# Performance work log

Hardware: AMD Instinct MI355X
Metric: run time of the kernel (lower is better)

## Reference

```python
import jax, jax.numpy as jnp
import numpy as np

N = 33_554_432
NUM_CLASSES = 10


def setup_inputs() -> dict:
    key = jax.random.key(0)
    k1, k2, k3 = jax.random.split(key, 3)
    predictions = jax.random.normal(k1, (N,), dtype=jnp.float32)
    labels = jax.random.randint(k2, (N,), 0, NUM_CLASSES, dtype=jnp.int32)
    weights = jax.random.uniform(k3, (NUM_CLASSES,), dtype=jnp.float32)
    return {"predictions": predictions, "labels": labels, "weights": weights}


def reference(predictions, labels, weights):
    # per-element weighted squared error: weights[label] * (pred - label)^2, then mean
    diff = predictions - labels.astype(predictions.dtype)
    w = weights[labels]  # gather per-class weight
    return jnp.mean(w * diff * diff)
```

## Files before the change

kernel.cpp:

```cpp
#include <hip/hip_runtime.h>

#define NBLOCKS 2048
#define NTHREADS 256
#define PER_THREAD 16
#define BATCH 4

__global__ __launch_bounds__(NTHREADS) void wmse_kernel(
    const float4* __restrict__ pred4,
    const int4* __restrict__ lab4,
    const float* __restrict__ weights,
    float* __restrict__ out,
    int n4, double inv_n)
{
    __shared__ float w[16];
    if (threadIdx.x < 10) w[threadIdx.x] = weights[threadIdx.x];
    __syncthreads();

    const int stride = NBLOCKS * NTHREADS;
    const int base = blockIdx.x * NTHREADS + threadIdx.x;

    double acc = 0.0;

    if (n4 == stride * PER_THREAD) {
        #pragma unroll 1
        for (int b = 0; b < PER_THREAD / BATCH; ++b) {
            float4 p[BATCH];
            int4   l[BATCH];
            #pragma unroll
            for (int k = 0; k < BATCH; ++k) {
                int i = base + (b * BATCH + k) * stride;
                p[k] = pred4[i];
                l[k] = lab4[i];
            }
            float s = 0.f;
            #pragma unroll
            for (int k = 0; k < BATCH; ++k) {
                float d0 = p[k].x - (float)l[k].x;
                float d1 = p[k].y - (float)l[k].y;
                float d2 = p[k].z - (float)l[k].z;
                float d3 = p[k].w - (float)l[k].w;
                s += w[l[k].x] * d0 * d0;
                s += w[l[k].y] * d1 * d1;
                s += w[l[k].z] * d2 * d2;
                s += w[l[k].w] * d3 * d3;
            }
            acc += (double)s;
        }
    } else {
        for (int i = base; i < n4; i += stride) {
            float4 p = pred4[i];
            int4 l = lab4[i];
            float d0 = p.x - (float)l.x;
            float d1 = p.y - (float)l.y;
            float d2 = p.z - (float)l.z;
            float d3 = p.w - (float)l.w;
            float s = w[l.x] * d0 * d0
                    + w[l.y] * d1 * d1
                    + w[l.z] * d2 * d2
                    + w[l.w] * d3 * d3;
            acc += (double)s;
        }
    }

    for (int off = 32; off > 0; off >>= 1)
        acc += __shfl_down(acc, off, 64);

    __shared__ double wave_sums[NTHREADS / 64];
    int lane = threadIdx.x & 63;
    int wid  = threadIdx.x >> 6;
    if (lane == 0) wave_sums[wid] = acc;
    __syncthreads();

    if (threadIdx.x == 0) {
        double t = 0.0;
        #pragma unroll
        for (int k = 0; k < NTHREADS / 64; ++k) t += wave_sums[k];
        atomicAdd(out, (float)(t * inv_n));
    }
}

extern "C" void kernel_launch(void* const* d_in, const int* in_sizes, int n_in,
                              void* d_out, int out_size, void* d_ws, size_t ws_size,
                              hipStream_t stream) {
    const float* pred    = (const float*)d_in[0];
    const int*   labels  = (const int*)d_in[1];
    const float* weights = (const float*)d_in[2];
    float* out = (float*)d_out;

    int n  = in_sizes[0];
    int n4 = n >> 2;

    hipMemsetAsync(out, 0, out_size * sizeof(float), stream);

    wmse_kernel<<<NBLOCKS, NTHREADS, 0, stream>>>(
        (const float4*)pred, (const int4*)labels, weights, out,
        n4, 1.0 / (double)n);
}
```

Before: 282.1 us.

## Use nontemporal loads, double grid size, and issue all eight loads upfront

Doubles the block count to 4096 so each thread handles 8 vector groups instead of 16. All 16 vector loads (predictions and labels) are issued at once before any compute, replacing the old batches of 4. The fast path now uses nontemporal loads so the streamed data does not pollute the caches. The aim is more memory-level parallelism and higher bandwidth for this streaming reduction, at the cost of more registers and twice as many block-level atomics.

```diff
diff --git a/kernel.cpp b/kernel.cpp
--- a/kernel.cpp
+++ b/kernel.cpp
@@ -1,13 +1,22 @@
 #include <hip/hip_runtime.h>
 
-#define NBLOCKS 2048
+#define NBLOCKS 4096
 #define NTHREADS 256
-#define PER_THREAD 16
-#define BATCH 4
+#define GROUPS 8
+
+typedef float fvec4 __attribute__((ext_vector_type(4)));
+typedef int   ivec4 __attribute__((ext_vector_type(4)));
+
+__device__ __forceinline__ fvec4 ntloadf(const fvec4* p) {
+    return __builtin_nontemporal_load(p);
+}
+__device__ __forceinline__ ivec4 ntloadi(const ivec4* p) {
+    return __builtin_nontemporal_load(p);
+}
 
 __global__ __launch_bounds__(NTHREADS) void wmse_kernel(
-    const float4* __restrict__ pred4,
-    const int4* __restrict__ lab4,
+    const fvec4* __restrict__ pred4,
+    const ivec4* __restrict__ lab4,
     const float* __restrict__ weights,
     float* __restrict__ out,
     int n4, double inv_n)
@@ -17,48 +26,42 @@
     __syncthreads();
 
     const int stride = NBLOCKS * NTHREADS;
-    const int base = blockIdx.x * NTHREADS + threadIdx.x;
+    const int t = blockIdx.x * NTHREADS + threadIdx.x;
 
     double acc = 0.0;
 
-    if (n4 == stride * PER_THREAD) {
-        #pragma unroll 1
-        for (int b = 0; b < PER_THREAD / BATCH; ++b) {
-            float4 p[BATCH];
-            int4   l[BATCH];
-            #pragma unroll
-            for (int k = 0; k < BATCH; ++k) {
-                int i = base + (b * BATCH + k) * stride;
-                p[k] = pred4[i];
-                l[k] = lab4[i];
-            }
-            float s = 0.f;
-            #pragma unroll
-            for (int k = 0; k < BATCH; ++k) {
-                float d0 = p[k].x - (float)l[k].x;
-                float d1 = p[k].y - (float)l[k].y;
-                float d2 = p[k].z - (float)l[k].z;
-                float d3 = p[k].w - (float)l[k].w;
-                s += w[l[k].x] * d0 * d0;
-                s += w[l[k].y] * d1 * d1;
-                s += w[l[k].z] * d2 * d2;
-                s += w[l[k].w] * d3 * d3;
-            }
-            acc += (double)s;
+    if (n4 == stride * GROUPS) {
+        fvec4 p[GROUPS];
+        ivec4 l[GROUPS];
+        #pragma unroll
+        for (int k = 0; k < GROUPS; ++k) {
+            p[k] = ntloadf(pred4 + t + k * stride);
+            l[k] = ntloadi(lab4 + t + k * stride);
+        }
+        #pragma unroll
+        for (int k = 0; k < GROUPS; k += 2) {
+            float d0 = p[k].x - (float)l[k].x;
+            float d1 = p[k].y - (float)l[k].y;
+            float d2 = p[k].z - (float)l[k].z;
+            float d3 = p[k].w - (float)l[k].w;
+            float sA = w[l[k].x]*d0*d0 + w[l[k].y]*d1*d1
+                     + w[l[k].z]*d2*d2 + w[l[k].w]*d3*d3;
+            float e0 = p[k+1].x - (float)l[k+1].x;
+            float e1 = p[k+1].y - (float)l[k+1].y;
+            float e2 = p[k+1].z - (float)l[k+1].z;
+            float e3 = p[k+1].w - (float)l[k+1].w;
+            float sB = w[l[k+1].x]*e0*e0 + w[l[k+1].y]*e1*e1
+                     + w[l[k+1].z]*e2*e2 + w[l[k+1].w]*e3*e3;
+            acc += (double)(sA + sB);
         }
     } else {
-        for (int i = base; i < n4; i += stride) {
-            float4 p = pred4[i];
-            int4 l = lab4[i];
-            float d0 = p.x - (float)l.x;
-            float d1 = p.y - (float)l.y;
-            float d2 = p.z - (float)l.z;
-            float d3 = p.w - (float)l.w;
-            float s = w[l.x] * d0 * d0
-                    + w[l.y] * d1 * d1
-                    + w[l.z] * d2 * d2
-                    + w[l.w] * d3 * d3;
-            acc += (double)s;
+        for (int i = t; i < n4; i += stride) {
+            fvec4 p = pred4[i];
+            ivec4 l = lab4[i];
+            float d0 = p.x - (float)l.x, d1 = p.y - (float)l.y;
+            float d2 = p.z - (float)l.z, d3 = p.w - (float)l.w;
+            acc += (double)(w[l.x]*d0*d0 + w[l.y]*d1*d1
+                          + w[l.z]*d2*d2 + w[l.w]*d3*d3);
         }
     }
 
@@ -72,10 +75,10 @@
     __syncthreads();
 
     if (threadIdx.x == 0) {
-        double t = 0.0;
+        double tsum = 0.0;
         #pragma unroll
-        for (int k = 0; k < NTHREADS / 64; ++k) t += wave_sums[k];
-        atomicAdd(out, (float)(t * inv_n));
+        for (int k = 0; k < NTHREADS / 64; ++k) tsum += wave_sums[k];
+        atomicAdd(out, (float)(tsum * inv_n));
     }
 }
 
@@ -93,6 +96,6 @@
     hipMemsetAsync(out, 0, out_size * sizeof(float), stream);
 
     wmse_kernel<<<NBLOCKS, NTHREADS, 0, stream>>>(
-        (const float4*)pred, (const int4*)labels, weights, out,
+        (const fvec4*)pred, (const ivec4*)labels, weights, out,
         n4, 1.0 / (double)n);
 }
```

Result: faster. 276.2 us (-2.1%).
